# Kernel tuning notes

Measured on AMD Instinct MI355X. Metric: run time of the kernel, lower is better.

## Reference

```python
import jax, jax.numpy as jnp
import numpy as np

T, B, NI = 100, 2048, 3
NU = 128          # nh_lstm
NB = 256          # nh_bottleneck
NPC, NHD = 256, 12
INIT = NPC + NHD  # 268


def setup_inputs() -> dict:
    key = jax.random.key(0)
    ks = jax.random.split(key, 20)
    s_in = 1.0 / np.sqrt(NI)
    s_u = 1.0 / np.sqrt(NU)
    s_b = 1.0 / np.sqrt(NB)
    s_e = 1.0 / np.sqrt(INIT)
    return {
        "x": jax.random.normal(ks[0], (T, B, NI), jnp.float32),
        "init_pc": jax.random.normal(ks[1], (B, NPC), jnp.float32),
        "init_hd": jax.random.normal(ks[2], (B, NHD), jnp.float32),
        "Wz": jax.random.normal(ks[3], (NI, NU), jnp.float32) * s_in,
        "Wr": jax.random.normal(ks[4], (NI, NU), jnp.float32) * s_in,
        "Wh": jax.random.normal(ks[5], (NI, NU), jnp.float32) * s_in,
        "Uz": jax.random.normal(ks[6], (NU, NU), jnp.float32) * s_u,
        "Ur": jax.random.normal(ks[7], (NU, NU), jnp.float32) * s_u,
        "Uh": jax.random.normal(ks[8], (NU, NU), jnp.float32) * s_u,
        "bz": jnp.zeros((NU,), jnp.float32),
        "br": jnp.zeros((NU,), jnp.float32),
        "bh": jnp.zeros((NU,), jnp.float32),
        "W_embed": jax.random.normal(ks[9], (INIT, NU), jnp.float32) * s_e,
        "b_embed": jnp.zeros((NU,), jnp.float32),
        "W_bneck": jax.random.normal(ks[10], (NU, NB), jnp.float32) * s_u,  # no bias
        "W_pc": jax.random.normal(ks[11], (NB, NPC), jnp.float32) * s_b,
        "b_pc": jnp.zeros((NPC,), jnp.float32),
        "W_hd": jax.random.normal(ks[12], (NB, NHD), jnp.float32) * s_b,
        "b_hd": jnp.zeros((NHD,), jnp.float32),
    }


def reference(x, init_pc, init_hd, Wz, Wr, Wh, Uz, Ur, Uh, bz, br, bh,
              W_embed, b_embed, W_bneck, W_pc, b_pc, W_hd, b_hd):
    # state_embed(cat(initial_conds))
    init = jnp.concatenate([init_pc, init_hd], axis=1)      # [B, 268]
    h0 = init @ W_embed + b_embed                           # [B, NU]

    # hoist input projections out of the recurrence: [T, B, NU]
    xz = x @ Wz + bz
    xr = x @ Wr + br
    xh = x @ Wh + bh

    def step(h, xs):
        xz_t, xr_t, xh_t = xs
        z = jax.nn.sigmoid(xz_t + h @ Uz)
        r = jax.nn.sigmoid(xr_t + h @ Ur)
        h_tw = jnp.tanh(xh_t + (r * h) @ Uh)
        h = (1.0 - z) * h + z * h_tw
        return h, h

    final_state, states = jax.lax.scan(step, h0, (xz, xr, xh))  # states: [T, B, NU]

    # bottleneck (dropout in eval mode = identity) and logit heads, batched over T
    bottleneck = states @ W_bneck                           # [T, B, NB]
    logits_pc = bottleneck @ W_pc + b_pc                    # [T, B, NPC]
    logits_hd = bottleneck @ W_hd + b_hd                    # [T, B, NHD]
    return logits_hd, logits_pc, bottleneck, states, final_state
```

## Files before the change

kernel.cpp:

```cpp
#include <hip/hip_runtime.h>

#define TT 100
#define BB 2048
#define NI 3
#define NU 128
#define NB 256
#define NPC 256
#define NHD 12

typedef __attribute__((ext_vector_type(8))) short short8;
typedef __attribute__((ext_vector_type(4))) float f32x4;

__device__ __forceinline__ float fast_sigmoid(float x) {
  return 1.0f / (1.0f + __expf(-x));
}
__device__ __forceinline__ float fast_tanh(float x) {
  return 1.0f - 2.0f / (__expf(2.0f * x) + 1.0f);
}
__device__ __forceinline__ short f2bf(float f) {
  uint32_t u = __float_as_uint(f);
  u += 0x7FFF + ((u >> 16) & 1);
  return (short)(u >> 16);
}
__device__ __forceinline__ float bf2f(short s) {
  return __uint_as_float(((uint32_t)(uint16_t)s) << 16);
}
__device__ __forceinline__ void lds_barrier() {
  asm volatile("s_waitcnt lgkmcnt(0)" ::: "memory");
  __builtin_amdgcn_s_barrier();
}

__global__ __launch_bounds__(256) void embed_kernel(
    const float* __restrict__ init_pc, const float* __restrict__ init_hd,
    const float* __restrict__ W_embed, const float* __restrict__ b_embed,
    float* __restrict__ h0) {
  __shared__ float pcs[2][NPC];
  __shared__ float hds[2][NHD];
  const int tid = threadIdx.x;
  const int b0 = blockIdx.x * 2;

  for (int idx = tid; idx < 2 * NPC; idx += 256)
    pcs[idx >> 8][idx & 255] =
        init_pc[(size_t)(b0 + (idx >> 8)) * NPC + (idx & 255)];
  if (tid < 2 * NHD) {
    int rr = tid / NHD, cc = tid - rr * NHD;
    hds[rr][cc] = init_hd[(size_t)(b0 + rr) * NHD + cc];
  }
  __syncthreads();

  const int half = tid >> 7;
  const int j = tid & 127;
  const float* Wp = W_embed + j;
  float a0 = 0.f, a1 = 0.f, a2 = 0.f, a3 = 0.f;
#pragma unroll 4
  for (int k = 0; k < NPC; k += 4) {
    a0 = fmaf(pcs[half][k + 0], Wp[(k + 0) * NU], a0);
    a1 = fmaf(pcs[half][k + 1], Wp[(k + 1) * NU], a1);
    a2 = fmaf(pcs[half][k + 2], Wp[(k + 2) * NU], a2);
    a3 = fmaf(pcs[half][k + 3], Wp[(k + 3) * NU], a3);
  }
#pragma unroll
  for (int k = 0; k < NHD; ++k)
    a0 = fmaf(hds[half][k], Wp[(NPC + k) * NU], a0);
  float acc = b_embed[j] + ((a0 + a1) + (a2 + a3));
  h0[(size_t)(b0 + half) * NU + j] = acc;
}

__global__ __launch_bounds__(512, 2) void gru_mfma_kernel(
    const float* __restrict__ x, const float* __restrict__ h0,
    const float* __restrict__ Wz, const float* __restrict__ Wr,
    const float* __restrict__ Wh, const float* __restrict__ Uz,
    const float* __restrict__ Ur, const float* __restrict__ Uh,
    const float* __restrict__ bz, const float* __restrict__ br,
    const float* __restrict__ bh, float* __restrict__ states,
    float* __restrict__ final_state) {
  __shared__ short h_hi[16 * 128];
  __shared__ short h_lo[16 * 128];
  __shared__ short p_hi[16 * 128];
  __shared__ short p_lo[16 * 128];
  __shared__ float xs[TT][8][4];

  const int tid = threadIdx.x;
  const int lane = tid & 63;
  const int w = tid >> 6;
  const int ln15 = lane & 15;
  const int g4 = lane >> 4;
  const int col = w * 16 + ln15;
  const int row0 = blockIdx.x * 8;

  for (int idx = tid; idx < TT * 32; idx += 512) {
    const int t = idx >> 5, rem = idx & 31, r = rem >> 2, i = rem & 3;
    xs[t][r][i] = (i < 3) ? x[(size_t)(t * BB + row0 + r) * NI + i] : 0.0f;
  }

  const float wz0 = Wz[col], wz1 = Wz[NU + col], wz2 = Wz[2 * NU + col];
  const float wr0 = Wr[col], wr1 = Wr[NU + col], wr2 = Wr[2 * NU + col];
  const float wh0 = Wh[col], wh1 = Wh[NU + col], wh2 = Wh[2 * NU + col];
  const float bzv = bz[col], brv = br[col], bhv = bh[col];

  short8 Uzh[4], Uzl[4], Urh[4], Url[4], Uhh[4], Uhl[4];
#pragma unroll
  for (int kt = 0; kt < 4; ++kt) {
#pragma unroll
    for (int e = 0; e < 8; ++e) {
      const int kk = kt * 32 + g4 * 8 + e;
      float v;
      short hi;
      v = Uz[kk * NU + col];
      hi = f2bf(v);
      Uzh[kt][e] = hi;
      Uzl[kt][e] = f2bf(v - bf2f(hi));
      v = Ur[kk * NU + col];
      hi = f2bf(v);
      Urh[kt][e] = hi;
      Url[kt][e] = f2bf(v - bf2f(hi));
      v = Uh[kk * NU + col];
      hi = f2bf(v);
      Uhh[kt][e] = hi;
      Uhl[kt][e] = f2bf(v - bf2f(hi));
    }
  }

  int foff[4];
#pragma unroll
  for (int kt = 0; kt < 4; ++kt)
    foff[kt] = ln15 * 256 + ((kt * 64 + g4 * 16) ^ ((ln15 & 7) << 4));
  int woff[4];
#pragma unroll
  for (int q = 0; q < 4; ++q) {
    const int row = g4 * 4 + q;
    woff[q] = row * 256 + ((col * 2) ^ ((row & 7) << 4));
  }

  float hreg[4];
#pragma unroll
  for (int q = 0; q < 4; ++q) {
    const int row = g4 * 4 + q;
    hreg[q] = (row < 8) ? h0[(size_t)(row0 + row) * NU + col] : 0.0f;
    const short hi = f2bf(hreg[q]);
    *(short*)((char*)h_hi + woff[q]) = hi;
    *(short*)((char*)h_lo + woff[q]) = f2bf(hreg[q] - bf2f(hi));
  }
  __syncthreads();

  float zg[4];

  for (int t = 0; t < TT; ++t) {
    {
      short8 ahi[4], alo[4];
#pragma unroll
      for (int kt = 0; kt < 4; ++kt) {
        ahi[kt] = *(const short8*)((const char*)h_hi + foff[kt]);
        alo[kt] = *(const short8*)((const char*)h_lo + foff[kt]);
      }
      float4 xrow[4];
#pragma unroll
      for (int q = 0; q < 4; ++q)
        xrow[q] = *(const float4*)xs[t][(g4 * 4 + q) & 7];

      f32x4 za, zb = {0.f, 0.f, 0.f, 0.f}, zc = {0.f, 0.f, 0.f, 0.f};
      f32x4 ra, rb = {0.f, 0.f, 0.f, 0.f}, rc = {0.f, 0.f, 0.f, 0.f};
#pragma unroll
      for (int q = 0; q < 4; ++q) {
        za[q] = fmaf(xrow[q].x, wz0,
                     fmaf(xrow[q].y, wz1, fmaf(xrow[q].z, wz2, bzv)));
        ra[q] = fmaf(xrow[q].x, wr0,
                     fmaf(xrow[q].y, wr1, fmaf(xrow[q].z, wr2, brv)));
      }
#pragma unroll
      for (int kt = 0; kt < 4; ++kt) {
        za = __builtin_amdgcn_mfma_f32_16x16x32_bf16(ahi[kt], Uzh[kt], za, 0, 0, 0);
        ra = __builtin_amdgcn_mfma_f32_16x16x32_bf16(ahi[kt], Urh[kt], ra, 0, 0, 0);
        zb = __builtin_amdgcn_mfma_f32_16x16x32_bf16(alo[kt], Uzh[kt], zb, 0, 0, 0);
        rb = __builtin_amdgcn_mfma_f32_16x16x32_bf16(alo[kt], Urh[kt], rb, 0, 0, 0);
        zc = __builtin_amdgcn_mfma_f32_16x16x32_bf16(ahi[kt], Uzl[kt], zc, 0, 0, 0);
        rc = __builtin_amdgcn_mfma_f32_16x16x32_bf16(ahi[kt], Url[kt], rc, 0, 0, 0);
      }
#pragma unroll
      for (int q = 0; q < 4; ++q)
        zg[q] = fast_sigmoid(za[q] + zb[q] + zc[q]);
      if (g4 < 2) {
#pragma unroll
        for (int q = 0; q < 4; ++q) {
          const float rh = fast_sigmoid(ra[q] + rb[q] + rc[q]) * hreg[q];
          const short hi = f2bf(rh);
          *(short*)((char*)p_hi + woff[q]) = hi;
          *(short*)((char*)p_lo + woff[q]) = f2bf(rh - bf2f(hi));
        }
      }
    }
    lds_barrier();

    {
      short8 phi[4], plo[4];
#pragma unroll
      for (int kt = 0; kt < 4; ++kt) {
        phi[kt] = *(const short8*)((const char*)p_hi + foff[kt]);
        plo[kt] = *(const short8*)((const char*)p_lo + foff[kt]);
      }
      float4 xrow[4];
#pragma unroll
      for (int q = 0; q < 4; ++q)
        xrow[q] = *(const float4*)xs[t][(g4 * 4 + q) & 7];

      f32x4 ha, hb = {0.f, 0.f, 0.f, 0.f}, hc = {0.f, 0.f, 0.f, 0.f};
#pragma unroll
      for (int q = 0; q < 4; ++q)
        ha[q] = fmaf(xrow[q].x, wh0,
                     fmaf(xrow[q].y, wh1, fmaf(xrow[q].z, wh2, bhv)));
#pragma unroll
      for (int kt = 0; kt < 4; ++kt) {
        ha = __builtin_amdgcn_mfma_f32_16x16x32_bf16(phi[kt], Uhh[kt], ha, 0, 0, 0);
        hb = __builtin_amdgcn_mfma_f32_16x16x32_bf16(plo[kt], Uhh[kt], hb, 0, 0, 0);
        hc = __builtin_amdgcn_mfma_f32_16x16x32_bf16(phi[kt], Uhl[kt], hc, 0, 0, 0);
      }
#pragma unroll
      for (int q = 0; q < 4; ++q) {
        const float htw = fast_tanh(ha[q] + hb[q] + hc[q]);
        hreg[q] = fmaf(zg[q], htw - hreg[q], hreg[q]);
      }
      if (g4 < 2) {
#pragma unroll
        for (int q = 0; q < 4; ++q)
          states[((size_t)t * BB + row0 + g4 * 4 + q) * NU + col] = hreg[q];
#pragma unroll
        for (int q = 0; q < 4; ++q) {
          const short hi = f2bf(hreg[q]);
          *(short*)((char*)h_hi + woff[q]) = hi;
          *(short*)((char*)h_lo + woff[q]) = f2bf(hreg[q] - bf2f(hi));
        }
      }
    }
    lds_barrier();
  }

  if (g4 < 2) {
#pragma unroll
    for (int q = 0; q < 4; ++q)
      final_state[(size_t)(row0 + g4 * 4 + q) * NU + col] = hreg[q];
  }
}

__global__ __launch_bounds__(256) void prepack_kernel(
    const float* __restrict__ Wb, const float* __restrict__ Wpc,
    const float* __restrict__ Whd, short* __restrict__ Wb_pack,
    short* __restrict__ Wpc_pack, short* __restrict__ Whd_pack) {
  int t = blockIdx.x * 256 + threadIdx.x;
  if (t >= 200 * 64) return;
  int fb = t >> 6, lane = t & 63;
  const float* W;
  short* out;
  int n_tile, k_tile, N, local;
  if (fb < 64) {
    W = Wb; out = Wb_pack; local = fb; n_tile = fb >> 2; k_tile = fb & 3; N = 256;
  } else if (fb < 192) {
    int f = fb - 64;
    W = Wpc; out = Wpc_pack; local = f; n_tile = f >> 3; k_tile = f & 7; N = 256;
  } else {
    int f = fb - 192;
    W = Whd; out = Whd_pack; local = f; n_tile = 0; k_tile = f; N = 12;
  }
  short8 p;
#pragma unroll
  for (int e = 0; e < 8; ++e) {
    int k = k_tile * 32 + (lane >> 4) * 8 + e;
    int colc = n_tile * 16 + (lane & 15);
    float v = (colc < N) ? W[k * N + colc] : 0.0f;
    p[e] = f2bf(v);
  }
  *((short8*)out + (local * 64 + lane)) = p;
}

__global__ __launch_bounds__(256, 3) void heads_mfma_kernel(
    const float* __restrict__ states, const short* __restrict__ Wb_pack,
    const short* __restrict__ Wpc_pack, const short* __restrict__ Whd_pack,
    const float* __restrict__ b_pc, const float* __restrict__ b_hd,
    float* __restrict__ out_hd, float* __restrict__ out_pc,
    float* __restrict__ out_bn) {
  __shared__ short s_lds[64 * 128];
  __shared__ short bn_lds[64 * 256];
  const int tid = threadIdx.x;
  const size_t R0 = (size_t)blockIdx.x * 64;

  for (int c = tid; c < 1024; c += 256) {
    int row = c >> 4, s16 = c & 15;
    const float* src = states + (R0 + row) * 128 + s16 * 8;
    float4 v0 = *(const float4*)src;
    float4 v1 = *(const float4*)(src + 4);
    short8 p;
    p[0] = f2bf(v0.x); p[1] = f2bf(v0.y); p[2] = f2bf(v0.z); p[3] = f2bf(v0.w);
    p[4] = f2bf(v1.x); p[5] = f2bf(v1.y); p[6] = f2bf(v1.z); p[7] = f2bf(v1.w);
    int byte = row * 256 + ((s16 * 16) ^ ((row & 7) << 4));
    *(short8*)((char*)s_lds + byte) = p;
  }
  __syncthreads();

  const int lane = tid & 63;
  const int wave = tid >> 6;
  const int ln15 = lane & 15;
  const int ln4 = lane >> 4;
  const int r0 = wave * 16;

  {
    short8 a[4];
#pragma unroll
    for (int kt = 0; kt < 4; ++kt) {
      int byte =
          (r0 + ln15) * 256 + ((kt * 64 + ln4 * 16) ^ ((ln15 & 7) << 4));
      a[kt] = *(const short8*)((const char*)s_lds + byte);
    }
#pragma unroll
    for (int nt = 0; nt < 16; ++nt) {
      f32x4 acc = {0.f, 0.f, 0.f, 0.f};
      const short8* bp = (const short8*)Wb_pack + (nt * 4) * 64 + lane;
#pragma unroll
      for (int kt = 0; kt < 4; ++kt)
        acc = __builtin_amdgcn_mfma_f32_16x16x32_bf16(a[kt], bp[kt * 64], acc,
                                                      0, 0, 0);
      int colc = nt * 16 + ln15;
#pragma unroll
      for (int q = 0; q < 4; ++q) {
        int row = r0 + ln4 * 4 + q;
        out_bn[(R0 + row) * NB + colc] = acc[q];
        int byte = row * 512 + ((colc * 2) ^ ((row & 7) << 4));
        *(short*)((char*)bn_lds + byte) = f2bf(acc[q]);
      }
    }
  }
  __syncthreads();

  {
    short8 ab[8];
#pragma unroll
    for (int kt = 0; kt < 8; ++kt) {
      int byte =
          (r0 + ln15) * 512 + ((kt * 64 + ln4 * 16) ^ ((ln15 & 7) << 4));
      ab[kt] = *(const short8*)((const char*)bn_lds + byte);
    }
#pragma unroll
    for (int nt = 0; nt < 16; ++nt) {
      int colc = nt * 16 + ln15;
      float bias = b_pc[colc];
      f32x4 acc = {bias, bias, bias, bias};
      const short8* bp = (const short8*)Wpc_pack + (nt * 8) * 64 + lane;
#pragma unroll
      for (int kt = 0; kt < 8; ++kt)
        acc = __builtin_amdgcn_mfma_f32_16x16x32_bf16(ab[kt], bp[kt * 64], acc,
                                                      0, 0, 0);
#pragma unroll
      for (int q = 0; q < 4; ++q)
        out_pc[(R0 + r0 + ln4 * 4 + q) * NPC + colc] = acc[q];
    }
    {
      int colc = ln15;
      float bias = (colc < NHD) ? b_hd[colc] : 0.0f;
      f32x4 acc = {bias, bias, bias, bias};
      const short8* bp = (const short8*)Whd_pack + lane;
#pragma unroll
      for (int kt = 0; kt < 8; ++kt)
        acc = __builtin_amdgcn_mfma_f32_16x16x32_bf16(ab[kt], bp[kt * 64], acc,
                                                      0, 0, 0);
      if (colc < NHD) {
#pragma unroll
        for (int q = 0; q < 4; ++q)
          out_hd[(R0 + r0 + ln4 * 4 + q) * NHD + colc] = acc[q];
      }
    }
  }
}

extern "C" void kernel_launch(void* const* d_in, const int* in_sizes, int n_in,
                              void* d_out, int out_size, void* d_ws,
                              size_t ws_size, hipStream_t stream) {
  (void)in_sizes;
  (void)n_in;
  (void)out_size;
  (void)ws_size;
  const float* x = (const float*)d_in[0];
  const float* init_pc = (const float*)d_in[1];
  const float* init_hd = (const float*)d_in[2];
  const float* Wz = (const float*)d_in[3];
  const float* Wr = (const float*)d_in[4];
  const float* Wh = (const float*)d_in[5];
  const float* Uz = (const float*)d_in[6];
  const float* Ur = (const float*)d_in[7];
  const float* Uh = (const float*)d_in[8];
  const float* bz = (const float*)d_in[9];
  const float* br = (const float*)d_in[10];
  const float* bh = (const float*)d_in[11];
  const float* W_embed = (const float*)d_in[12];
  const float* b_embed = (const float*)d_in[13];
  const float* W_bneck = (const float*)d_in[14];
  const float* W_pc = (const float*)d_in[15];
  const float* b_pc = (const float*)d_in[16];
  const float* W_hd = (const float*)d_in[17];
  const float* b_hd = (const float*)d_in[18];

  float* out = (float*)d_out;
  float* out_hd = out;
  float* out_pc = out_hd + (size_t)TT * BB * NHD;
  float* out_bn = out_pc + (size_t)TT * BB * NPC;
  float* out_st = out_bn + (size_t)TT * BB * NB;
  float* out_fs = out_st + (size_t)TT * BB * NU;

  float* h0 = (float*)d_ws;
  short* Wb_pack = (short*)((char*)d_ws + (1 << 20));
  short* Wpc_pack = Wb_pack + 64 * 64 * 8;
  short* Whd_pack = Wpc_pack + 128 * 64 * 8;

  prepack_kernel<<<50, 256, 0, stream>>>(W_bneck, W_pc, W_hd, Wb_pack,
                                         Wpc_pack, Whd_pack);
  embed_kernel<<<BB / 2, 256, 0, stream>>>(init_pc, init_hd, W_embed, b_embed,
                                           h0);
  gru_mfma_kernel<<<BB / 8, 512, 0, stream>>>(x, h0, Wz, Wr, Wh, Uz, Ur, Uh,
                                              bz, br, bh, out_st, out_fs);
  heads_mfma_kernel<<<(TT * BB) / 64, 256, 0, stream>>>(
      out_st, Wb_pack, Wpc_pack, Whd_pack, b_pc, b_hd, out_hd, out_pc, out_bn);
}
```

Measured before the change: 388.6 us.

## Rewrite GRU scan as single-wave blocks with LDS-resident prepacked weight fragments

Replaces the 8-wave GRU block, which handled 8 batch rows and needed two block barriers per timestep, with a single-wave block that handles 16 rows and all 128 columns. The wave needs no barriers, and every MFMA row is now real data instead of half being padding. A new prepack kernel converts the recurrent weights into bf16 hi/lo MFMA fragments once. The hi fragments and the input-projection fragments are kept in about 120KB of LDS, and the Uh lo fragments stay in registers. The x-projection and bias are folded into an extra MFMA using a bf16 input fragment, which lowers the precision of that term. Grid size falls to 128 blocks of 64 threads, so each CU runs very few waves and one wave serialises all the MFMAs of a timestep.

```diff
diff --git a/kernel.cpp b/kernel.cpp
--- a/kernel.cpp
+++ b/kernel.cpp
@@ -11,6 +11,11 @@
 typedef __attribute__((ext_vector_type(8))) short short8;
 typedef __attribute__((ext_vector_type(4))) float f32x4;
 
+#define GRU_FRAG_BYTES (120 * 1024)
+#define GRU_PLANES_OFF GRU_FRAG_BYTES
+#define GRU_XT_OFF (GRU_FRAG_BYTES + 16 * 1024)
+#define GRU_LDS_BYTES (GRU_XT_OFF + 2 * 16 * 4 * 4)
+
 __device__ __forceinline__ float fast_sigmoid(float x) {
   return 1.0f / (1.0f + __expf(-x));
 }
@@ -24,10 +29,6 @@
 }
 __device__ __forceinline__ float bf2f(short s) {
   return __uint_as_float(((uint32_t)(uint16_t)s) << 16);
-}
-__device__ __forceinline__ void lds_barrier() {
-  asm volatile("s_waitcnt lgkmcnt(0)" ::: "memory");
-  __builtin_amdgcn_s_barrier();
 }
 
 __global__ __launch_bounds__(256) void embed_kernel(
@@ -66,179 +67,212 @@
   h0[(size_t)(b0 + half) * NU + j] = acc;
 }
 
-__global__ __launch_bounds__(512, 2) void gru_mfma_kernel(
+__global__ __launch_bounds__(256) void prepack_gru_kernel(
+    const float* __restrict__ Uz, const float* __restrict__ Ur,
+    const float* __restrict__ Uh, const float* __restrict__ Wz,
+    const float* __restrict__ Wr, const float* __restrict__ Wh,
+    const float* __restrict__ bz, const float* __restrict__ br,
+    const float* __restrict__ bh, short* __restrict__ gfrags) {
+  int t = blockIdx.x * 256 + threadIdx.x;
+  if (t >= 152 * 64) return;
+  const int f = t >> 6, lane = t & 63;
+  const int ln15 = lane & 15, g4 = lane >> 4;
+  short8 p;
+  if (f < 128) {
+    const int g = f >> 5;
+    const int nt = (f >> 2) & 7, kt = f & 3;
+    const float* U = (g == 0) ? Uz : (g == 1) ? Ur : Uh;
+#pragma unroll
+    for (int e = 0; e < 8; ++e) {
+      const float v = U[(kt * 32 + g4 * 8 + e) * NU + nt * 16 + ln15];
+      const short hi = f2bf(v);
+      p[e] = (f < 96) ? hi : f2bf(v - bf2f(hi));
+    }
+  } else {
+    const int w = f - 128;
+    const int g = w >> 3, nt = w & 7;
+    const float* W = (g == 0) ? Wz : (g == 1) ? Wr : Wh;
+    const float* bb = (g == 0) ? bz : (g == 1) ? br : bh;
+    const int col = nt * 16 + ln15;
+#pragma unroll
+    for (int e = 0; e < 8; ++e) {
+      const int k = g4 * 8 + e;
+      float v = 0.0f;
+      if (k < 3) v = W[k * NU + col];
+      if (k == 3) v = bb[col];
+      p[e] = f2bf(v);
+    }
+  }
+  *((short8*)gfrags + (f * 64 + lane)) = p;
+}
+
+__global__ __launch_bounds__(64, 1) void gru_scan_kernel(
     const float* __restrict__ x, const float* __restrict__ h0,
-    const float* __restrict__ Wz, const float* __restrict__ Wr,
-    const float* __restrict__ Wh, const float* __restrict__ Uz,
-    const float* __restrict__ Ur, const float* __restrict__ Uh,
-    const float* __restrict__ bz, const float* __restrict__ br,
-    const float* __restrict__ bh, float* __restrict__ states,
+    const short* __restrict__ gfrags, float* __restrict__ states,
     float* __restrict__ final_state) {
-  __shared__ short h_hi[16 * 128];
-  __shared__ short h_lo[16 * 128];
-  __shared__ short p_hi[16 * 128];
-  __shared__ short p_lo[16 * 128];
-  __shared__ float xs[TT][8][4];
-
-  const int tid = threadIdx.x;
-  const int lane = tid & 63;
-  const int w = tid >> 6;
-  const int ln15 = lane & 15;
-  const int g4 = lane >> 4;
-  const int col = w * 16 + ln15;
-  const int row0 = blockIdx.x * 8;
-
-  for (int idx = tid; idx < TT * 32; idx += 512) {
-    const int t = idx >> 5, rem = idx & 31, r = rem >> 2, i = rem & 3;
-    xs[t][r][i] = (i < 3) ? x[(size_t)(t * BB + row0 + r) * NI + i] : 0.0f;
-  }
-
-  const float wz0 = Wz[col], wz1 = Wz[NU + col], wz2 = Wz[2 * NU + col];
-  const float wr0 = Wr[col], wr1 = Wr[NU + col], wr2 = Wr[2 * NU + col];
-  const float wh0 = Wh[col], wh1 = Wh[NU + col], wh2 = Wh[2 * NU + col];
-  const float bzv = bz[col], brv = br[col], bhv = bh[col];
-
-  short8 Uzh[4], Uzl[4], Urh[4], Url[4], Uhh[4], Uhl[4];
-#pragma unroll
-  for (int kt = 0; kt < 4; ++kt) {
-#pragma unroll
-    for (int e = 0; e < 8; ++e) {
-      const int kk = kt * 32 + g4 * 8 + e;
-      float v;
-      short hi;
-      v = Uz[kk * NU + col];
-      hi = f2bf(v);
-      Uzh[kt][e] = hi;
-      Uzl[kt][e] = f2bf(v - bf2f(hi));
-      v = Ur[kk * NU + col];
-      hi = f2bf(v);
-      Urh[kt][e] = hi;
-      Url[kt][e] = f2bf(v - bf2f(hi));
-      v = Uh[kk * NU + col];
-      hi = f2bf(v);
-      Uhh[kt][e] = hi;
-      Uhl[kt][e] = f2bf(v - bf2f(hi));
-    }
-  }
+  extern __shared__ char smem[];
+  const short8* fr = (const short8*)smem;
+  char* h_hi = smem + GRU_PLANES_OFF;
+  char* h_lo = h_hi + 4096;
+  char* p_hi = h_lo + 4096;
+  char* p_lo = p_hi + 4096;
+  float* xt = (float*)(smem + GRU_XT_OFF);
+
+  const int lane = threadIdx.x;
+  const int ln15 = lane & 15, g4 = lane >> 4;
+  const int row0 = blockIdx.x * 16;
+
+  {
+    short8* dst = (short8*)smem;
+    for (int i = lane; i < 120 * 64; i += 64) {
+      const int slot = i >> 6;
+      const int src = (slot < 96) ? slot : slot + 32;
+      dst[i] = *(const short8*)(gfrags + ((size_t)src * 64 + (i & 63)) * 8);
+    }
+  }
+
+  short8 Ulo[8][4];
+#pragma unroll
+  for (int nt = 0; nt < 8; ++nt)
+#pragma unroll
+    for (int kt = 0; kt < 4; ++kt)
+      Ulo[nt][kt] =
+          *(const short8*)(gfrags + ((size_t)(96 + nt * 4 + kt) * 64 + lane) * 8);
 
   int foff[4];
 #pragma unroll
   for (int kt = 0; kt < 4; ++kt)
     foff[kt] = ln15 * 256 + ((kt * 64 + g4 * 16) ^ ((ln15 & 7) << 4));
-  int woff[4];
-#pragma unroll
-  for (int q = 0; q < 4; ++q) {
-    const int row = g4 * 4 + q;
-    woff[q] = row * 256 + ((col * 2) ^ ((row & 7) << 4));
-  }
-
-  float hreg[4];
-#pragma unroll
-  for (int q = 0; q < 4; ++q) {
-    const int row = g4 * 4 + q;
-    hreg[q] = (row < 8) ? h0[(size_t)(row0 + row) * NU + col] : 0.0f;
-    const short hi = f2bf(hreg[q]);
-    *(short*)((char*)h_hi + woff[q]) = hi;
-    *(short*)((char*)h_lo + woff[q]) = f2bf(hreg[q] - bf2f(hi));
-  }
-  __syncthreads();
-
-  float zg[4];
-
+
+  float hreg[8][4];
+#pragma unroll
+  for (int nt = 0; nt < 8; ++nt)
+#pragma unroll
+    for (int q = 0; q < 4; ++q) {
+      const int row = g4 * 4 + q;
+      const float v = h0[(size_t)(row0 + row) * NU + nt * 16 + ln15];
+      hreg[nt][q] = v;
+      const int byte =
+          row * 256 + (((nt * 16 + ln15) * 2) ^ ((row & 7) << 4));
+      const short hi = f2bf(v);
+      *(short*)(h_hi + byte) = hi;
+      *(short*)(h_lo + byte) = f2bf(v - bf2f(hi));
+    }
+
+  if (lane < 48) {
+    const int r = lane / 3, i = lane - r * 3;
+    xt[0 * 64 + r * 4 + i] = x[(size_t)(row0 + r) * NI + i];
+  }
+
+#pragma unroll 1
   for (int t = 0; t < TT; ++t) {
+    const int pb = t & 1;
+
+    short8 ahi[4], alo[4];
+#pragma unroll
+    for (int kt = 0; kt < 4; ++kt) {
+      ahi[kt] = *(const short8*)(h_hi + foff[kt]);
+      alo[kt] = *(const short8*)(h_lo + foff[kt]);
+    }
+    short8 ax = {0, 0, 0, 0, 0, 0, 0, 0};
     {
-      short8 ahi[4], alo[4];
+      const float4 xv = *(const float4*)&xt[pb * 64 + ln15 * 4];
+      if (g4 == 0) {
+        ax[0] = f2bf(xv.x);
+        ax[1] = f2bf(xv.y);
+        ax[2] = f2bf(xv.z);
+        ax[3] = (short)0x3F80;
+      }
+    }
+    float xnext = 0.0f;
+    int xr = 0, xi = 0;
+    if (t + 1 < TT && lane < 48) {
+      xr = lane / 3;
+      xi = lane - xr * 3;
+      xnext = x[(size_t)((t + 1) * BB + row0 + xr) * NI + xi];
+    }
+
+    f32x4 zacc[8], racc[8];
+#pragma unroll
+    for (int nt = 0; nt < 8; ++nt) {
+      const f32x4 zz = {0.f, 0.f, 0.f, 0.f};
+      f32x4 z = __builtin_amdgcn_mfma_f32_16x16x32_bf16(
+          ax, fr[(96 + nt) * 64 + lane], zz, 0, 0, 0);
+      f32x4 r = __builtin_amdgcn_mfma_f32_16x16x32_bf16(
+          ax, fr[(104 + nt) * 64 + lane], zz, 0, 0, 0);
+      const short8* Bz = fr + (0 * 32 + nt * 4) * 64 + lane;
+      const short8* Br = fr + (1 * 32 + nt * 4) * 64 + lane;
 #pragma unroll
       for (int kt = 0; kt < 4; ++kt) {
-        ahi[kt] = *(const short8*)((const char*)h_hi + foff[kt]);
-        alo[kt] = *(const short8*)((const char*)h_lo + foff[kt]);
-      }
-      float4 xrow[4];
-#pragma unroll
-      for (int q = 0; q < 4; ++q)
-        xrow[q] = *(const float4*)xs[t][(g4 * 4 + q) & 7];
-
-      f32x4 za, zb = {0.f, 0.f, 0.f, 0.f}, zc = {0.f, 0.f, 0.f, 0.f};
-      f32x4 ra, rb = {0.f, 0.f, 0.f, 0.f}, rc = {0.f, 0.f, 0.f, 0.f};
+        const short8 b_z = Bz[kt * 64];
+        const short8 b_r = Br[kt * 64];
+        z = __builtin_amdgcn_mfma_f32_16x16x32_bf16(ahi[kt], b_z, z, 0, 0, 0);
+        r = __builtin_amdgcn_mfma_f32_16x16x32_bf16(ahi[kt], b_r, r, 0, 0, 0);
+        z = __builtin_amdgcn_mfma_f32_16x16x32_bf16(alo[kt], b_z, z, 0, 0, 0);
+        r = __builtin_amdgcn_mfma_f32_16x16x32_bf16(alo[kt], b_r, r, 0, 0, 0);
+      }
+      zacc[nt] = z;
+      racc[nt] = r;
+    }
+
+#pragma unroll
+    for (int nt = 0; nt < 8; ++nt)
 #pragma unroll
       for (int q = 0; q < 4; ++q) {
-        za[q] = fmaf(xrow[q].x, wz0,
-                     fmaf(xrow[q].y, wz1, fmaf(xrow[q].z, wz2, bzv)));
-        ra[q] = fmaf(xrow[q].x, wr0,
-                     fmaf(xrow[q].y, wr1, fmaf(xrow[q].z, wr2, brv)));
-      }
+        const int row = g4 * 4 + q;
+        const float rh = fast_sigmoid(racc[nt][q]) * hreg[nt][q];
+        const short hi = f2bf(rh);
+        const int byte =
+            row * 256 + (((nt * 16 + ln15) * 2) ^ ((row & 7) << 4));
+        *(short*)(p_hi + byte) = hi;
+        *(short*)(p_lo + byte) = f2bf(rh - bf2f(hi));
+        zacc[nt][q] = fast_sigmoid(zacc[nt][q]);
+      }
+
+    short8 phi[4], plo[4];
+#pragma unroll
+    for (int kt = 0; kt < 4; ++kt) {
+      phi[kt] = *(const short8*)(p_hi + foff[kt]);
+      plo[kt] = *(const short8*)(p_lo + foff[kt]);
+    }
+#pragma unroll
+    for (int nt = 0; nt < 8; ++nt) {
+      const f32x4 zz = {0.f, 0.f, 0.f, 0.f};
+      f32x4 h = __builtin_amdgcn_mfma_f32_16x16x32_bf16(
+          ax, fr[(112 + nt) * 64 + lane], zz, 0, 0, 0);
+      const short8* Bh = fr + (2 * 32 + nt * 4) * 64 + lane;
 #pragma unroll
       for (int kt = 0; kt < 4; ++kt) {
-        za = __builtin_amdgcn_mfma_f32_16x16x32_bf16(ahi[kt], Uzh[kt], za, 0, 0, 0);
-        ra = __builtin_amdgcn_mfma_f32_16x16x32_bf16(ahi[kt], Urh[kt], ra, 0, 0, 0);
-        zb = __builtin_amdgcn_mfma_f32_16x16x32_bf16(alo[kt], Uzh[kt], zb, 0, 0, 0);
-        rb = __builtin_amdgcn_mfma_f32_16x16x32_bf16(alo[kt], Urh[kt], rb, 0, 0, 0);
-        zc = __builtin_amdgcn_mfma_f32_16x16x32_bf16(ahi[kt], Uzl[kt], zc, 0, 0, 0);
-        rc = __builtin_amdgcn_mfma_f32_16x16x32_bf16(ahi[kt], Url[kt], rc, 0, 0, 0);
-      }
-#pragma unroll
-      for (int q = 0; q < 4; ++q)
-        zg[q] = fast_sigmoid(za[q] + zb[q] + zc[q]);
-      if (g4 < 2) {
-#pragma unroll
-        for (int q = 0; q < 4; ++q) {
-          const float rh = fast_sigmoid(ra[q] + rb[q] + rc[q]) * hreg[q];
-          const short hi = f2bf(rh);
-          *(short*)((char*)p_hi + woff[q]) = hi;
-          *(short*)((char*)p_lo + woff[q]) = f2bf(rh - bf2f(hi));
-        }
-      }
-    }
-    lds_barrier();
-
-    {
-      short8 phi[4], plo[4];
-#pragma unroll
-      for (int kt = 0; kt < 4; ++kt) {
-        phi[kt] = *(const short8*)((const char*)p_hi + foff[kt]);
-        plo[kt] = *(const short8*)((const char*)p_lo + foff[kt]);
-      }
-      float4 xrow[4];
-#pragma unroll
-      for (int q = 0; q < 4; ++q)
-        xrow[q] = *(const float4*)xs[t][(g4 * 4 + q) & 7];
-
-      f32x4 ha, hb = {0.f, 0.f, 0.f, 0.f}, hc = {0.f, 0.f, 0.f, 0.f};
-#pragma unroll
-      for (int q = 0; q < 4; ++q)
-        ha[q] = fmaf(xrow[q].x, wh0,
-                     fmaf(xrow[q].y, wh1, fmaf(xrow[q].z, wh2, bhv)));
-#pragma unroll
-      for (int kt = 0; kt < 4; ++kt) {
-        ha = __builtin_amdgcn_mfma_f32_16x16x32_bf16(phi[kt], Uhh[kt], ha, 0, 0, 0);
-        hb = __builtin_amdgcn_mfma_f32_16x16x32_bf16(plo[kt], Uhh[kt], hb, 0, 0, 0);
-        hc = __builtin_amdgcn_mfma_f32_16x16x32_bf16(phi[kt], Uhl[kt], hc, 0, 0, 0);
+        const short8 b_h = Bh[kt * 64];
+        h = __builtin_amdgcn_mfma_f32_16x16x32_bf16(phi[kt], b_h, h, 0, 0, 0);
+        h = __builtin_amdgcn_mfma_f32_16x16x32_bf16(plo[kt], b_h, h, 0, 0, 0);
+        h = __builtin_amdgcn_mfma_f32_16x16x32_bf16(phi[kt], Ulo[nt][kt], h, 0,
+                                                    0, 0);
       }
 #pragma unroll
       for (int q = 0; q < 4; ++q) {
-        const float htw = fast_tanh(ha[q] + hb[q] + hc[q]);
-        hreg[q] = fmaf(zg[q], htw - hreg[q], hreg[q]);
-      }
-      if (g4 < 2) {
-#pragma unroll
-        for (int q = 0; q < 4; ++q)
-          states[((size_t)t * BB + row0 + g4 * 4 + q) * NU + col] = hreg[q];
-#pragma unroll
-        for (int q = 0; q < 4; ++q) {
-          const short hi = f2bf(hreg[q]);
-          *(short*)((char*)h_hi + woff[q]) = hi;
-          *(short*)((char*)h_lo + woff[q]) = f2bf(hreg[q] - bf2f(hi));
-        }
-      }
-    }
-    lds_barrier();
-  }
-
-  if (g4 < 2) {
+        const int row = g4 * 4 + q;
+        const float htw = fast_tanh(h[q]);
+        const float hnew = fmaf(zacc[nt][q], htw - hreg[nt][q], hreg[nt][q]);
+        hreg[nt][q] = hnew;
+        const int byte =
+            row * 256 + (((nt * 16 + ln15) * 2) ^ ((row & 7) << 4));
+        const short hi = f2bf(hnew);
+        *(short*)(h_hi + byte) = hi;
+        *(short*)(h_lo + byte) = f2bf(hnew - bf2f(hi));
+        states[((size_t)t * BB + row0 + row) * NU + nt * 16 + ln15] = hnew;
+      }
+    }
+
+    if (t + 1 < TT && lane < 48) xt[(pb ^ 1) * 64 + xr * 4 + xi] = xnext;
+  }
+
+#pragma unroll
+  for (int nt = 0; nt < 8; ++nt)
 #pragma unroll
     for (int q = 0; q < 4; ++q)
-      final_state[(size_t)(row0 + g4 * 4 + q) * NU + col] = hreg[q];
-  }
+      final_state[(size_t)(row0 + g4 * 4 + q) * NU + nt * 16 + ln15] =
+          hreg[nt][q];
 }
 
 __global__ __launch_bounds__(256) void prepack_kernel(
@@ -407,13 +441,20 @@
   short* Wb_pack = (short*)((char*)d_ws + (1 << 20));
   short* Wpc_pack = Wb_pack + 64 * 64 * 8;
   short* Whd_pack = Wpc_pack + 128 * 64 * 8;
+  short* gru_frags = (short*)((char*)d_ws + (1 << 20) + 200 * 1024);
+
+  hipFuncSetAttribute((const void*)gru_scan_kernel,
+                      hipFuncAttributeMaxDynamicSharedMemorySize,
+                      GRU_LDS_BYTES);
 
   prepack_kernel<<<50, 256, 0, stream>>>(W_bneck, W_pc, W_hd, Wb_pack,
                                          Wpc_pack, Whd_pack);
+  prepack_gru_kernel<<<38, 256, 0, stream>>>(Uz, Ur, Uh, Wz, Wr, Wh, bz, br,
+                                             bh, gru_frags);
   embed_kernel<<<BB / 2, 256, 0, stream>>>(init_pc, init_hd, W_embed, b_embed,
                                            h0);
-  gru_mfma_kernel<<<BB / 8, 512, 0, stream>>>(x, h0, Wz, Wr, Wh, Uz, Ur, Uh,
-                                              bz, br, bh, out_st, out_fs);
+  gru_scan_kernel<<<BB / 16, 64, GRU_LDS_BYTES, stream>>>(x, h0, gru_frags,
+                                                          out_st, out_fs);
   heads_mfma_kernel<<<(TT * BB) / 64, 256, 0, stream>>>(
       out_st, Wb_pack, Wpc_pack, Whd_pack, b_pc, b_hd, out_hd, out_pc, out_bn);
 }
```

Result: slower. 1.153 ms (+196.7%).
